# Performance work log

Hardware: AMD Instinct MI355X
Metric: run time of the kernel (lower is better)

Reference implementation:

```python
import jax, jax.numpy as jnp
import numpy as np

DICE_W, BCE_W = 1.0, 1.0
BBOX_W = 0.025
L1_W, GIOU_W = 1.0, 1.0  # assumed BoxLoss weighting: loss = l1.sum(-1) + (1 - giou)


def _xywh_to_xyxy(b):
    cx, cy, w, h = b[..., 0], b[..., 1], b[..., 2], b[..., 3]
    return jnp.stack([cx - w / 2, cy - h / 2, cx + w / 2, cy + h / 2], axis=-1)


def _xyxy_to_xywh(b):
    x1, y1, x2, y2 = b[..., 0], b[..., 1], b[..., 2], b[..., 3]
    return jnp.stack([(x1 + x2) / 2, (y1 + y2) / 2, x2 - x1, y2 - y1], axis=-1)


def _giou(a, b):
    # a, b: [N,4] xyxy, paired GIoU
    ix1 = jnp.maximum(a[:, 0], b[:, 0]); iy1 = jnp.maximum(a[:, 1], b[:, 1])
    ix2 = jnp.minimum(a[:, 2], b[:, 2]); iy2 = jnp.minimum(a[:, 3], b[:, 3])
    inter = jnp.clip(ix2 - ix1, 0) * jnp.clip(iy2 - iy1, 0)
    area_a = jnp.clip(a[:, 2] - a[:, 0], 0) * jnp.clip(a[:, 3] - a[:, 1], 0)
    area_b = jnp.clip(b[:, 2] - b[:, 0], 0) * jnp.clip(b[:, 3] - b[:, 1], 0)
    union = area_a + area_b - inter
    iou = inter / jnp.maximum(union, 1e-6)
    cx1 = jnp.minimum(a[:, 0], b[:, 0]); cy1 = jnp.minimum(a[:, 1], b[:, 1])
    cx2 = jnp.maximum(a[:, 2], b[:, 2]); cy2 = jnp.maximum(a[:, 3], b[:, 3])
    c = jnp.clip(cx2 - cx1, 0) * jnp.clip(cy2 - cy1, 0)
    return iou - (c - union) / jnp.maximum(c, 1e-6)


def _box_loss_per_sample(pred_xywh, tgt_xywh):
    l1 = jnp.abs(pred_xywh - tgt_xywh).sum(-1)
    g = 1.0 - _giou(_xywh_to_xyxy(pred_xywh), _xywh_to_xyxy(tgt_xywh))
    return L1_W * l1 + GIOU_W * g


def _forward(pred_mask, pred_bbox, gt_bbox_rand, target_mask, img_h, img_w):
    B = pred_mask.shape[0]
    H, W = img_h, img_w
    tgt = target_mask.astype(pred_mask.dtype)          # [B,H,W] binary
    logits = pred_mask[:, 0]                           # [B,H,W]
    probs = jax.nn.sigmoid(logits)

    # ---- seg_loss: dice + bce (both mean-reduced) ----
    p = probs.reshape(B, -1); t = tgt.reshape(B, -1)
    dice = 1.0 - (2.0 * (p * t).sum(1) + 1.0) / (p.sum(1) + t.sum(1) + 1.0)
    x = logits.reshape(B, -1)
    bce = jnp.maximum(x, 0) - x * t + jnp.log1p(jnp.exp(-jnp.abs(x)))
    loss_mask = DICE_W * dice.mean() + BCE_W * bce.mean()

    # ---- bbox_loss: gt x1y1x2y2 (pixels) -> normalized cxcywh ----
    gx1 = gt_bbox_rand[:, 0] * (0.45 * W); gy1 = gt_bbox_rand[:, 1] * (0.45 * H)
    gx2 = gx1 + 1.0 + gt_bbox_rand[:, 2] * (0.5 * W)
    gy2 = gy1 + 1.0 + gt_bbox_rand[:, 3] * (0.5 * H)
    gt_xyxy = jnp.stack([gx1, gy1, gx2, gy2], axis=-1)
    # original divides by img_size [H,W] repeated -> [H,W,H,W] (square imgs)
    norm_div = jnp.asarray([H, W, H, W], dtype=pred_bbox.dtype)
    gt_norm = _xyxy_to_xywh(gt_xyxy) / norm_div
    loss_det = _box_loss_per_sample(pred_bbox, gt_norm).mean() * BBOX_W

    # ---- boxseg_iouloss2 (vectorized over the per-batch python loop) ----
    box_xyxy = _xywh_to_xyxy(pred_bbox)                # normalized xyxy
    scale = jnp.asarray([W, H, W, H], dtype=pred_bbox.dtype)
    pix = (box_xyxy * scale).astype(jnp.int32)         # trunc like .to(int)
    x1p = jnp.clip(pix[:, 0], 0, W); x2p = jnp.clip(pix[:, 2], 0, W)
    y1p = jnp.clip(pix[:, 1], 0, H); y2p = jnp.clip(pix[:, 3], 0, H)
    seg_bin = (probs > 0.5).astype(pred_mask.dtype)    # S2Bthr == B2Sthr == 0.5
    xs = jnp.arange(W); ys = jnp.arange(H)
    in_x = (xs[None, :] >= x1p[:, None]) & (xs[None, :] < x2p[:, None])  # [B,W]
    in_y = (ys[None, :] >= y1p[:, None]) & (ys[None, :] < y2p[:, None])  # [B,H]
    inside = in_y[:, :, None] & in_x[:, None, :]                          # [B,H,W]
    inter = (seg_bin * inside).sum((1, 2))
    area = seg_bin.sum((1, 2))
    s2b_iou = jnp.where(area > 0, inter / jnp.maximum(area, 1.0), 0.0)
    loss_s2b = (1.0 - s2b_iou).mean()

    # get_maskouterbox: per-sample min/max of coords where mask is on
    mb = seg_bin.astype(bool)
    x1o = jnp.min(jnp.where(mb, xs[None, None, :], W), axis=(1, 2))
    y1o = jnp.min(jnp.where(mb, ys[None, :, None], H), axis=(1, 2))
    x2o = jnp.max(jnp.where(mb, xs[None, None, :], -1), axis=(1, 2))
    y2o = jnp.max(jnp.where(mb, ys[None, :, None], -1), axis=(1, 2))
    present = (area > 0)[:, None]
    outer = jnp.stack([x1o, y1o, x2o, y2o], axis=-1).astype(pred_bbox.dtype)
    outer = jnp.where(present, outer, 0.0) / scale
    loss_b2s = _box_loss_per_sample(_xyxy_to_xywh(outer), _xyxy_to_xywh(box_xyxy)).mean()

    return loss_mask + loss_det + loss_s2b + loss_b2s


def setup_inputs() -> dict:
    key = jax.random.key(0)
    k1, k2, k3, k4 = jax.random.split(key, 4)
    B, H, W = 64, 512, 512
    return {
        "pred_mask": jax.random.normal(k1, (B, 1, H, W), dtype=jnp.float32),
        "pred_bbox": jax.random.uniform(k2, (B, 4), dtype=jnp.float32),
        "gt_bbox_rand": jax.random.uniform(k3, (B, 4), dtype=jnp.float32),
        "target_mask": jax.random.randint(k4, (B, H, W), 0, 2, dtype=jnp.int32),
        "img_h": H,
        "img_w": W,
    }


def reference(pred_mask, pred_bbox, gt_bbox_rand, target_mask, img_h, img_w):
    return _forward(pred_mask, pred_bbox, gt_bbox_rand, target_mask, img_h, img_w)
```

## Files before the change

### kernel.cpp

```cpp
#include <hip/hip_runtime.h>
#include <math.h>


#define BPS 16
#define TPB 256

__device__ inline float box_loss_xywh(const float pb[4], const float tb[4]) {
    float l1 = fabsf(pb[0] - tb[0]) + fabsf(pb[1] - tb[1]) +
               fabsf(pb[2] - tb[2]) + fabsf(pb[3] - tb[3]);
    float ax1 = pb[0] - 0.5f * pb[2], ay1 = pb[1] - 0.5f * pb[3];
    float ax2 = pb[0] + 0.5f * pb[2], ay2 = pb[1] + 0.5f * pb[3];
    float bx1 = tb[0] - 0.5f * tb[2], by1 = tb[1] - 0.5f * tb[3];
    float bx2 = tb[0] + 0.5f * tb[2], by2 = tb[1] + 0.5f * tb[3];

    float ix1 = fmaxf(ax1, bx1), iy1 = fmaxf(ay1, by1);
    float ix2 = fminf(ax2, bx2), iy2 = fminf(ay2, by2);
    float inter  = fmaxf(ix2 - ix1, 0.f) * fmaxf(iy2 - iy1, 0.f);
    float area_a = fmaxf(ax2 - ax1, 0.f) * fmaxf(ay2 - ay1, 0.f);
    float area_b = fmaxf(bx2 - bx1, 0.f) * fmaxf(by2 - by1, 0.f);
    float uni = area_a + area_b - inter;
    float iou = inter / fmaxf(uni, 1e-6f);
    float cx1 = fminf(ax1, bx1), cy1 = fminf(ay1, by1);
    float cx2 = fmaxf(ax2, bx2), cy2 = fmaxf(ay2, by2);
    float c = fmaxf(cx2 - cx1, 0.f) * fmaxf(cy2 - cy1, 0.f);
    float giou = iou - (c - uni) / fmaxf(c, 1e-6f);
    return l1 + (1.0f - giou);
}

__global__ __launch_bounds__(TPB)
void uh_reduce(const float* __restrict__ pred_mask,
               const int*   __restrict__ target_mask,
               const float* __restrict__ pred_bbox,
               const int*   __restrict__ pH, const int* __restrict__ pW,
               float* __restrict__ wf, int* __restrict__ wi,
               int HW, int N)
{
    const int b     = blockIdx.y;
    const int chunk = blockIdx.x;
    const int W = *pW;
    const int H = *pH;

    __shared__ int sbox[4];
    if (threadIdx.x == 0) {
        float c0 = pred_bbox[b * 4 + 0], c1 = pred_bbox[b * 4 + 1];
        float c2 = pred_bbox[b * 4 + 2], c3 = pred_bbox[b * 4 + 3];
        float x1 = (c0 - 0.5f * c2) * (float)W;
        float y1 = (c1 - 0.5f * c3) * (float)H;
        float x2 = (c0 + 0.5f * c2) * (float)W;
        float y2 = (c1 + 0.5f * c3) * (float)H;
        sbox[0] = min(max((int)x1, 0), W);
        sbox[1] = min(max((int)y1, 0), H);
        sbox[2] = min(max((int)x2, 0), W);
        sbox[3] = min(max((int)y2, 0), H);
    }
    __syncthreads();
    const int bx1 = sbox[0], by1 = sbox[1], bx2 = sbox[2], by2 = sbox[3];

    const int  chunk_px = HW / BPS;
    const long base = (long)b * HW + (long)chunk * chunk_px;

    float s_pt = 0.f, s_p = 0.f, s_bce = 0.f;
    int c_t = 0, c_area = 0, c_inter = 0;
    int xmn = W, xmx = -1, ymn = H, ymx = -1;

    for (int i = threadIdx.x * 4; i < chunk_px; i += TPB * 4) {
        const int pix0 = chunk * chunk_px + i;
        float4 xv = *(const float4*)(pred_mask + base + i);
        int4   tv = *(const int4*)(target_mask + base + i);

        int y = pix0 / W;
        int x = pix0 - y * W;

        float xs4[4] = {xv.x, xv.y, xv.z, xv.w};
        int   ts4[4] = {tv.x, tv.y, tv.z, tv.w};
        #pragma unroll
        for (int j = 0; j < 4; ++j) {
            float xl = xs4[j];
            float tf = (float)ts4[j];
            float e  = __expf(-fabsf(xl));
            s_bce += fmaxf(xl, 0.f) - xl * tf + log1pf(e);
            float p = (xl >= 0.f) ? 1.f / (1.f + e) : e / (1.f + e);
            s_p  += p;
            s_pt += p * tf;
            c_t  += ts4[j];
            if (xl > 0.f) {
                ++c_area;
                xmn = min(xmn, x); xmx = max(xmx, x);
                ymn = min(ymn, y); ymx = max(ymx, y);
                c_inter += (x >= bx1 && x < bx2 && y >= by1 && y < by2) ? 1 : 0;
            }
            if (++x >= W) { x = 0; ++y; }
        }
    }

    #pragma unroll
    for (int o = 32; o; o >>= 1) {
        s_pt  += __shfl_down(s_pt,  o, 64);
        s_p   += __shfl_down(s_p,   o, 64);
        s_bce += __shfl_down(s_bce, o, 64);
        c_t    += __shfl_down(c_t,    o, 64);
        c_area += __shfl_down(c_area, o, 64);
        c_inter+= __shfl_down(c_inter,o, 64);
        xmn = min(xmn, __shfl_down(xmn, o, 64));
        ymn = min(ymn, __shfl_down(ymn, o, 64));
        xmx = max(xmx, __shfl_down(xmx, o, 64));
        ymx = max(ymx, __shfl_down(ymx, o, 64));
    }

    __shared__ float smf[3][4];
    __shared__ int   smi[7][4];
    const int wid = threadIdx.x >> 6;
    if ((threadIdx.x & 63) == 0) {
        smf[0][wid] = s_pt;  smf[1][wid] = s_p;  smf[2][wid] = s_bce;
        smi[0][wid] = c_t;   smi[1][wid] = c_area; smi[2][wid] = c_inter;
        smi[3][wid] = xmn;   smi[4][wid] = ymn;
        smi[5][wid] = xmx;   smi[6][wid] = ymx;
    }
    __syncthreads();
    if (threadIdx.x == 0) {
        float a0 = 0.f, a1 = 0.f, a2 = 0.f;
        int i0 = 0, i1 = 0, i2 = 0;
        int m3 = W, m4 = H, m5 = -1, m6 = -1;
        #pragma unroll
        for (int w = 0; w < 4; ++w) {
            a0 += smf[0][w]; a1 += smf[1][w]; a2 += smf[2][w];
            i0 += smi[0][w]; i1 += smi[1][w]; i2 += smi[2][w];
            m3 = min(m3, smi[3][w]); m4 = min(m4, smi[4][w]);
            m5 = max(m5, smi[5][w]); m6 = max(m6, smi[6][w]);
        }
        const int idx = b * BPS + chunk;
        wf[0 * N + idx] = a0; wf[1 * N + idx] = a1; wf[2 * N + idx] = a2;
        wi[0 * N + idx] = i0; wi[1 * N + idx] = i1; wi[2 * N + idx] = i2;
        wi[3 * N + idx] = m3; wi[4 * N + idx] = m4;
        wi[5 * N + idx] = m5; wi[6 * N + idx] = m6;
    }
}

__global__ __launch_bounds__(64)
void uh_final(const float* __restrict__ pred_bbox,
              const float* __restrict__ gt_bbox,
              const int* __restrict__ pH, const int* __restrict__ pW,
              const float* __restrict__ wf, const int* __restrict__ wi,
              int B, int HW, float* __restrict__ out)
{
    const int W = *pW, H = *pH;
    const int N = B * BPS;
    float v = 0.f;

    for (int b = threadIdx.x; b < B; b += 64) {
        float s_pt = 0.f, s_p = 0.f, s_bce = 0.f;
        int c_t = 0, c_area = 0, c_inter = 0;
        int xmn = W, ymn = H, xmx = -1, ymx = -1;
        for (int c = 0; c < BPS; ++c) {
            const int idx = b * BPS + c;
            s_pt  += wf[0 * N + idx];
            s_p   += wf[1 * N + idx];
            s_bce += wf[2 * N + idx];
            c_t    += wi[0 * N + idx];
            c_area += wi[1 * N + idx];
            c_inter+= wi[2 * N + idx];
            xmn = min(xmn, wi[3 * N + idx]); ymn = min(ymn, wi[4 * N + idx]);
            xmx = max(xmx, wi[5 * N + idx]); ymx = max(ymx, wi[6 * N + idx]);
        }

        float dice = 1.f - (2.f * s_pt + 1.f) / (s_p + (float)c_t + 1.f);

        float pb[4] = {pred_bbox[b*4+0], pred_bbox[b*4+1],
                       pred_bbox[b*4+2], pred_bbox[b*4+3]};
        float g0 = gt_bbox[b*4+0], g1 = gt_bbox[b*4+1];
        float g2 = gt_bbox[b*4+2], g3 = gt_bbox[b*4+3];
        float gx1 = g0 * (0.45f * (float)W);
        float gy1 = g1 * (0.45f * (float)H);
        float gx2 = gx1 + 1.0f + g2 * (0.5f * (float)W);
        float gy2 = gy1 + 1.0f + g3 * (0.5f * (float)H);
        float gt[4] = { ((gx1 + gx2) * 0.5f) / (float)H,
                        ((gy1 + gy2) * 0.5f) / (float)W,
                        (gx2 - gx1) / (float)H,
                        (gy2 - gy1) / (float)W };
        float det = 0.025f * box_loss_xywh(pb, gt);

        float iou_s2b = (c_area > 0)
                          ? (float)c_inter / fmaxf((float)c_area, 1.f) : 0.f;
        float s2b = 1.f - iou_s2b;

        float ox1, oy1, ox2, oy2;
        if (c_area > 0) {
            ox1 = (float)xmn; oy1 = (float)ymn;
            ox2 = (float)xmx; oy2 = (float)ymx;
        } else {
            ox1 = oy1 = ox2 = oy2 = 0.f;
        }
        ox1 /= (float)W; ox2 /= (float)W;
        oy1 /= (float)H; oy2 /= (float)H;
        float ow[4] = { (ox1 + ox2) * 0.5f, (oy1 + oy2) * 0.5f,
                        ox2 - ox1, oy2 - oy1 };
        float px1 = pb[0] - 0.5f * pb[2], py1 = pb[1] - 0.5f * pb[3];
        float px2 = pb[0] + 0.5f * pb[2], py2 = pb[1] + 0.5f * pb[3];
        float pw[4] = { (px1 + px2) * 0.5f, (py1 + py2) * 0.5f,
                        px2 - px1, py2 - py1 };
        float b2s = box_loss_xywh(ow, pw);

        v += dice + s_bce / (float)HW + det + s2b + b2s;
    }

    #pragma unroll
    for (int o = 32; o; o >>= 1) v += __shfl_down(v, o, 64);
    if (threadIdx.x == 0) out[0] = v / (float)B;
}

extern "C" void kernel_launch(void* const* d_in, const int* in_sizes, int n_in,
                              void* d_out, int out_size, void* d_ws, size_t ws_size,
                              hipStream_t stream) {
    const float* pred_mask   = (const float*)d_in[0];
    const float* pred_bbox   = (const float*)d_in[1];
    const float* gt_bbox     = (const float*)d_in[2];
    const int*   target_mask = (const int*)d_in[3];
    const int*   pH          = (const int*)d_in[4];
    const int*   pW          = (const int*)d_in[5];
    float* out = (float*)d_out;

    const int B  = in_sizes[1] / 4;
    const int HW = in_sizes[0] / B;
    const int N  = B * BPS;

    float* wf = (float*)d_ws;
    int*   wi = (int*)d_ws + (size_t)3 * N;

    dim3 grid(BPS, B);
    uh_reduce<<<grid, TPB, 0, stream>>>(pred_mask, target_mask, pred_bbox,
                                        pH, pW, wf, wi, HW, N);
    uh_final<<<1, 64, 0, stream>>>(pred_bbox, gt_bbox, pH, pW, wf, wi,
                                   B, HW, out);
}
```

Before: 180.4 us.

## Restructure mask reduction to row-aligned tiles with bitmask bbox extents

Each thread now owns a fixed 4-column slice and walks rows with a fixed stride, so x-inclusion tests are hoisted out of the loop and min/max extents come from row and column bitmasks resolved with ffs/clz after the loop. The sigmoid and softplus now share one hardware reciprocal and a fast log, replacing the divides and log1pf. Blocks per sample go from 16 to 32 when the workspace allows. The row bitmask assumes each chunk has at most 32 rows and that the shapes divide evenly, and the fast math may change precision slightly.

```diff
diff --git a/kernel.cpp b/kernel.cpp
--- a/kernel.cpp
+++ b/kernel.cpp
@@ -2,7 +2,6 @@
 #include <math.h>
 
 
-#define BPS 16
 #define TPB 256
 
 __device__ inline float box_loss_xywh(const float pb[4], const float tb[4]) {
@@ -35,8 +34,9 @@
                float* __restrict__ wf, int* __restrict__ wi,
                int HW, int N)
 {
-    const int b     = blockIdx.y;
-    const int chunk = blockIdx.x;
+    const int b      = blockIdx.y;
+    const int chunk  = blockIdx.x;
+    const int nchunk = gridDim.x;
     const int W = *pW;
     const int H = *pH;
 
@@ -56,41 +56,70 @@
     __syncthreads();
     const int bx1 = sbox[0], by1 = sbox[1], bx2 = sbox[2], by2 = sbox[3];
 
-    const int  chunk_px = HW / BPS;
-    const long base = (long)b * HW + (long)chunk * chunk_px;
+    const int chunk_px = HW / nchunk;
+    const int rows     = chunk_px / W;
+    const int tpr      = W >> 2;
+    const int rpi      = TPB / tpr;
+    const int iters    = rows / rpi;
+    const int rowoff   = threadIdx.x / tpr;
+    const int cx       = (threadIdx.x - rowoff * tpr) << 2;
+    const int ybase    = chunk * rows;
+
+    const int inx0 = (cx + 0 >= bx1) & (cx + 0 < bx2);
+    const int inx1 = (cx + 1 >= bx1) & (cx + 1 < bx2);
+    const int inx2 = (cx + 2 >= bx1) & (cx + 2 < bx2);
+    const int inx3 = (cx + 3 >= bx1) & (cx + 3 < bx2);
+
+    const long boff = (long)b * HW + (long)(ybase + rowoff) * W + cx;
+    const float* pp = pred_mask + boff;
+    const int*   tp = target_mask + boff;
+    const int    stride = rpi * W;
 
     float s_pt = 0.f, s_p = 0.f, s_bce = 0.f;
     int c_t = 0, c_area = 0, c_inter = 0;
-    int xmn = W, xmx = -1, ymn = H, ymx = -1;
-
-    for (int i = threadIdx.x * 4; i < chunk_px; i += TPB * 4) {
-        const int pix0 = chunk * chunk_px + i;
-        float4 xv = *(const float4*)(pred_mask + base + i);
-        int4   tv = *(const int4*)(target_mask + base + i);
-
-        int y = pix0 / W;
-        int x = pix0 - y * W;
-
-        float xs4[4] = {xv.x, xv.y, xv.z, xv.w};
-        int   ts4[4] = {tv.x, tv.y, tv.z, tv.w};
+    unsigned int rmask = 0, colmask = 0;
+    int yloc = rowoff;
+
+    for (int it = 0; it < iters; ++it) {
+        float4 xv = *(const float4*)pp;
+        int4   tv = *(const int4*)tp;
+        pp += stride; tp += stride;
+
+        float xs[4] = {xv.x, xv.y, xv.z, xv.w};
+        int   ts[4] = {tv.x, tv.y, tv.z, tv.w};
+        int pos[4];
         #pragma unroll
         for (int j = 0; j < 4; ++j) {
-            float xl = xs4[j];
-            float tf = (float)ts4[j];
+            float xl = xs[j];
+            float tf = (float)ts[j];
             float e  = __expf(-fabsf(xl));
-            s_bce += fmaxf(xl, 0.f) - xl * tf + log1pf(e);
-            float p = (xl >= 0.f) ? 1.f / (1.f + e) : e / (1.f + e);
+            float r  = __builtin_amdgcn_rcpf(1.f + e);
+            float p  = (xl >= 0.f) ? r : e * r;
+            s_bce += fmaxf(xl, 0.f) - xl * tf - __logf(r);
             s_p  += p;
-            s_pt += p * tf;
-            c_t  += ts4[j];
-            if (xl > 0.f) {
-                ++c_area;
-                xmn = min(xmn, x); xmx = max(xmx, x);
-                ymn = min(ymn, y); ymx = max(ymx, y);
-                c_inter += (x >= bx1 && x < bx2 && y >= by1 && y < by2) ? 1 : 0;
-            }
-            if (++x >= W) { x = 0; ++y; }
-        }
+            s_pt  = fmaf(p, tf, s_pt);
+            c_t  += ts[j];
+            pos[j] = xl > 0.f;
+        }
+        int anyp = pos[0] | pos[1] | pos[2] | pos[3];
+        c_area  += pos[0] + pos[1] + pos[2] + pos[3];
+        colmask |= (unsigned)(pos[0] | (pos[1] << 1) | (pos[2] << 2) | (pos[3] << 3));
+        rmask   |= (unsigned)anyp << yloc;
+        const int y = ybase + yloc;
+        const int inrow = (y >= by1) & (y < by2);
+        c_inter += inrow ? ((pos[0] & inx0) + (pos[1] & inx1) +
+                            (pos[2] & inx2) + (pos[3] & inx3)) : 0;
+        yloc += rpi;
+    }
+
+    int xmn = W, xmx = -1, ymn = H, ymx = -1;
+    if (colmask) {
+        xmn = cx + (__ffs(colmask) - 1);
+        xmx = cx + (31 - __clz(colmask));
+    }
+    if (rmask) {
+        ymn = ybase + (__ffs(rmask) - 1);
+        ymx = ybase + (31 - __clz(rmask));
     }
 
     #pragma unroll
@@ -128,7 +157,7 @@
             m3 = min(m3, smi[3][w]); m4 = min(m4, smi[4][w]);
             m5 = max(m5, smi[5][w]); m6 = max(m6, smi[6][w]);
         }
-        const int idx = b * BPS + chunk;
+        const int idx = b * nchunk + chunk;
         wf[0 * N + idx] = a0; wf[1 * N + idx] = a1; wf[2 * N + idx] = a2;
         wi[0 * N + idx] = i0; wi[1 * N + idx] = i1; wi[2 * N + idx] = i2;
         wi[3 * N + idx] = m3; wi[4 * N + idx] = m4;
@@ -141,18 +170,18 @@
               const float* __restrict__ gt_bbox,
               const int* __restrict__ pH, const int* __restrict__ pW,
               const float* __restrict__ wf, const int* __restrict__ wi,
-              int B, int HW, float* __restrict__ out)
+              int B, int HW, int nchunk, float* __restrict__ out)
 {
     const int W = *pW, H = *pH;
-    const int N = B * BPS;
+    const int N = B * nchunk;
     float v = 0.f;
 
     for (int b = threadIdx.x; b < B; b += 64) {
         float s_pt = 0.f, s_p = 0.f, s_bce = 0.f;
         int c_t = 0, c_area = 0, c_inter = 0;
         int xmn = W, ymn = H, xmx = -1, ymx = -1;
-        for (int c = 0; c < BPS; ++c) {
-            const int idx = b * BPS + c;
+        for (int c = 0; c < nchunk; ++c) {
+            const int idx = b * nchunk + c;
             s_pt  += wf[0 * N + idx];
             s_p   += wf[1 * N + idx];
             s_bce += wf[2 * N + idx];
@@ -221,14 +250,17 @@
 
     const int B  = in_sizes[1] / 4;
     const int HW = in_sizes[0] / B;
-    const int N  = B * BPS;
+
+    int bps = 32;
+    if ((size_t)10 * sizeof(int) * B * bps > ws_size) bps = 16;
+    const int N = B * bps;
 
     float* wf = (float*)d_ws;
     int*   wi = (int*)d_ws + (size_t)3 * N;
 
-    dim3 grid(BPS, B);
+    dim3 grid(bps, B);
     uh_reduce<<<grid, TPB, 0, stream>>>(pred_mask, target_mask, pred_bbox,
                                         pH, pW, wf, wi, HW, N);
     uh_final<<<1, 64, 0, stream>>>(pred_bbox, gt_bbox, pH, pW, wf, wi,
-                                   B, HW, out);
-}
+                                   B, HW, bps, out);
+}
```

After: 172.3 us. -4.5%, faster.
